# Optimization experiments

Hardware: AMD Instinct MI355X
Metric: run time of the kernel (lower is better)

The kernel has to match this reference:

```python
import jax, jax.numpy as jnp
import numpy as np


def _lstm(x, W_ih, W_hh, b_ih, b_hh):
    """PyTorch-semantics LSTM over [B, T, F] -> [B, T, H]. Gate order: i, f, g, o."""
    H = W_hh.shape[1]
    # Precompute input projection for all timesteps: [B, T, 4H]
    xg = jnp.einsum('btf,gf->btg', x, W_ih) + b_ih + b_hh
    xg = jnp.transpose(xg, (1, 0, 2))  # time-major [T, B, 4H]
    B = x.shape[0]
    h0 = jnp.zeros((B, H), dtype=x.dtype)
    c0 = jnp.zeros((B, H), dtype=x.dtype)

    def step(carry, xt):
        h, c = carry
        gates = xt + h @ W_hh.T  # [B, 4H]
        i, f, g, o = jnp.split(gates, 4, axis=-1)
        i = jax.nn.sigmoid(i)
        f = jax.nn.sigmoid(f)
        g = jnp.tanh(g)
        o = jax.nn.sigmoid(o)
        c = f * c + i * g
        h = o * jnp.tanh(c)
        return (h, c), h

    _, hs = jax.lax.scan(step, (h0, c0), xg)
    return jnp.transpose(hs, (1, 0, 2))  # [B, T, H]


def setup_inputs() -> dict:
    key = jax.random.key(0)
    ks = jax.random.split(key, 16)
    B, T, F = 4096, 256, 32
    H1, H2, D1 = 64, 32, 16
    s1 = 1.0 / np.sqrt(H1)
    s2 = 1.0 / np.sqrt(H2)
    inp = {
        'x': jax.random.normal(ks[0], (B, T, F), dtype=jnp.float32),
        'W_ih1': jax.random.uniform(ks[1], (4 * H1, F), jnp.float32, -s1, s1),
        'W_hh1': jax.random.uniform(ks[2], (4 * H1, H1), jnp.float32, -s1, s1),
        'b_ih1': jax.random.uniform(ks[3], (4 * H1,), jnp.float32, -s1, s1),
        'b_hh1': jax.random.uniform(ks[4], (4 * H1,), jnp.float32, -s1, s1),
        'W_ih2': jax.random.uniform(ks[5], (4 * H2, H1), jnp.float32, -s2, s2),
        'W_hh2': jax.random.uniform(ks[6], (4 * H2, H2), jnp.float32, -s2, s2),
        'b_ih2': jax.random.uniform(ks[7], (4 * H2,), jnp.float32, -s2, s2),
        'b_hh2': jax.random.uniform(ks[8], (4 * H2,), jnp.float32, -s2, s2),
        'W_fc1': jax.random.uniform(ks[9], (D1, H2), jnp.float32, -s2, s2),
        'b_fc1': jax.random.uniform(ks[10], (D1,), jnp.float32, -s2, s2),
        'W_fc2': jax.random.uniform(ks[11], (1, D1), jnp.float32, -0.25, 0.25),
        'b_fc2': jax.random.uniform(ks[12], (1,), jnp.float32, -0.25, 0.25),
    }
    return inp


def reference(x, W_ih1, W_hh1, b_ih1, b_hh1, W_ih2, W_hh2, b_ih2, b_hh2,
              W_fc1, b_fc1, W_fc2, b_fc2):
    # Dropout is identity in eval/inference mode.
    h = _lstm(x, W_ih1, W_hh1, b_ih1, b_hh1)        # [B, T, 64]
    h = _lstm(h, W_ih2, W_hh2, b_ih2, b_hh2)        # [B, T, 32]
    h = h[:, -1, :]                                  # [B, 32]
    h = jax.nn.relu(h @ W_fc1.T + b_fc1)             # [B, 16]
    out = h @ W_fc2.T + b_fc2                        # [B, 1]
    return out.squeeze(-1)                           # [B]
```

## Files before the change

kernel.cpp:

```cpp
#include <hip/hip_runtime.h>

#define T_   256
#define F_   32
#define NBB  16
#define TPB  768
#define IMW  136
#define XLW  40
#define PR1  260
#define PR2  132

typedef __attribute__((ext_vector_type(8))) short bf16x8;
typedef __attribute__((ext_vector_type(4))) float f32x4;
typedef __attribute__((ext_vector_type(4))) unsigned short ush4;

#define K1f  (-1.44269504f)
#define K2f  (-2.88539008f)

__device__ __forceinline__ unsigned short bf16_rne(float x){
    unsigned u = __float_as_uint(x);
    u += 0x7FFF + ((u >> 16) & 1);
    return (unsigned short)(u >> 16);
}
__device__ __forceinline__ void bf16_split(float x, unsigned short& h, unsigned short& l){
    h = bf16_rne(x);
    float xr = __uint_as_float(((unsigned)h) << 16);
    l = bf16_rne(x - xr);
}
__device__ __forceinline__ void make_frags_s(const float* __restrict__ p8, float s,
                                             bf16x8& fh, bf16x8& fl){
    #pragma unroll
    for (int e = 0; e < 8; ++e){
        unsigned short h, l; bf16_split(s * p8[e], h, l);
        fh[e] = (short)h; fl[e] = (short)l;
    }
}
__device__ __forceinline__ float sigm_pre(float p){
    return __builtin_amdgcn_rcpf(1.f + __builtin_amdgcn_exp2f(p));
}
__device__ __forceinline__ float tanh_pre(float p){
    return fmaf(2.f, __builtin_amdgcn_rcpf(1.f + __builtin_amdgcn_exp2f(p)), -1.f);
}
__device__ __forceinline__ float unit_combine(float gi, float gf, float gg, float go, float& c){
    const float i_ = sigm_pre(gi);
    const float f_ = sigm_pre(gf);
    const float g_ = tanh_pre(gg);
    const float o_ = sigm_pre(go);
    c = fmaf(f_, c, i_ * g_);
    return o_ * tanh_pre(K2f * c);
}

#define MFMA(A,B,C) __builtin_amdgcn_mfma_f32_16x16x32_bf16((A),(B),(C),0,0,0)

__device__ __forceinline__ void step_barrier(){
    asm volatile("s_waitcnt lgkmcnt(0)" ::: "memory");
    __builtin_amdgcn_s_barrier();
}

__global__ __launch_bounds__(TPB, 3) void lstm_mfma(
    const float* __restrict__ x,
    const float* __restrict__ W_ih1,
    const float* __restrict__ W_hh1,
    const float* __restrict__ b_ih1,
    const float* __restrict__ b_hh1,
    const float* __restrict__ W_ih2,
    const float* __restrict__ W_hh2,
    const float* __restrict__ b_ih2,
    const float* __restrict__ b_hh2,
    const float* __restrict__ W_fc1,
    const float* __restrict__ b_fc1,
    const float* __restrict__ W_fc2,
    const float* __restrict__ b_fc2,
    float* __restrict__ out)
{
    const int tid  = threadIdx.x;
    const int lane = tid & 63;
    const int wid  = tid >> 6;
    const int bb   = lane & 15;
    const int kg   = (lane >> 4) & 3;
    const int b0   = blockIdx.x * NBB;

    __shared__ __align__(16) unsigned short i12[2][NBB][IMW];
    __shared__ __align__(16) unsigned short x1l[2][NBB][XLW];
    __shared__ __align__(16) float pre1[NBB * PR1];
    __shared__ __align__(16) float pre2[NBB * PR2];
    __shared__ float hfin[NBB][32];
    __shared__ float hd[NBB][16];

    bf16x8 wh[2][3], wl[2][3];
    f32x4  bfr[2];
    int    offs[2];
    if (wid < 8){
        #pragma unroll
        for (int tt = 0; tt < 2; ++tt){
            const int Tt = 2*wid + tt;
            const int g = Tt >> 2, rb = Tt & 3;
            const float s = (g == 2) ? K2f : K1f;
            offs[tt] = 64*g + 16*rb;
            const int r = offs[tt] + bb;
            make_frags_s(&W_ih1[r*32 +      8*kg], s, wh[tt][0], wl[tt][0]);
            make_frags_s(&W_hh1[r*64 +      8*kg], s, wh[tt][1], wl[tt][1]);
            make_frags_s(&W_hh1[r*64 + 32 + 8*kg], s, wh[tt][2], wl[tt][2]);
            #pragma unroll
            for (int q = 0; q < 4; ++q){
                const int row = offs[tt] + 4*kg + q;
                bfr[tt][q] = s * (b_ih1[row] + b_hh1[row]);
            }
        }
    } else {
        const int j = wid - 8;
        #pragma unroll
        for (int tt = 0; tt < 2; ++tt){
            const int St = 2*j + tt;
            const int g = St >> 1, rb = St & 1;
            const float s = (g == 2) ? K2f : K1f;
            offs[tt] = 32*g + 16*rb;
            const int r = offs[tt] + bb;
            make_frags_s(&W_ih2[r*64 +      8*kg], s, wh[tt][0], wl[tt][0]);
            make_frags_s(&W_ih2[r*64 + 32 + 8*kg], s, wh[tt][1], wl[tt][1]);
            make_frags_s(&W_hh2[r*32 +      8*kg], s, wh[tt][2], wl[tt][2]);
            #pragma unroll
            for (int q = 0; q < 4; ++q){
                const int row = offs[tt] + 4*kg + q;
                bfr[tt][q] = s * (b_ih2[row] + b_hh2[row]);
            }
        }
    }

    const int cb = tid >> 4;
    const int u0 = (tid & 15) * 4;
    float c1[4] = {0.f, 0.f, 0.f, 0.f};
    const int c2t = tid & 127;
    const int cb2 = c2t >> 3;
    const int v0  = (c2t & 7) * 4;
    float c2[4] = {0.f, 0.f, 0.f, 0.f};
    const int xt  = tid & 127;
    const int xcb = xt >> 3;
    const int xf  = (xt & 7) * 4;
    const size_t xbase = (size_t)(b0 + xcb) * (T_*F_) + xf;
    float4 xc = make_float4(0.f, 0.f, 0.f, 0.f);

    for (int i = tid; i < 2*NBB*IMW; i += TPB) (&i12[0][0][0])[i] = 0;
    __syncthreads();
    if (wid >= 10){
        float4 x0 = *(const float4*)&x[xbase];
        ush4 HH, HL;
        unsigned short h, l;
        bf16_split(x0.x, h, l); HH[0]=h; HL[0]=l;
        bf16_split(x0.y, h, l); HH[1]=h; HL[1]=l;
        bf16_split(x0.z, h, l); HH[2]=h; HL[2]=l;
        bf16_split(x0.w, h, l); HH[3]=h; HL[3]=l;
        *(ush4*)&i12[0][xcb][xf] = HH;
        *(ush4*)&x1l[0][xcb][xf] = HL;
        xc = *(const float4*)&x[xbase + F_];
    }
    __syncthreads();

    for (int t = 0; t <= T_ + 1; ++t){
        const int cur = t & 1, nxt = cur ^ 1;

        if (wid < 8){
            if (t < T_){
                const unsigned short* ph = &i12[cur][0][0] + bb*IMW + 8*kg;
                bf16x8 vh[3];
                #pragma unroll
                for (int kb = 0; kb < 3; ++kb)
                    vh[kb] = *(const bf16x8*)(ph + 32*kb);
                const bf16x8 vl0 = *(const bf16x8*)&x1l[cur][bb][8*kg];
                __builtin_amdgcn_s_setprio(1);
                f32x4 a0 = bfr[0], a1 = bfr[1];
                #pragma unroll
                for (int kb = 0; kb < 3; ++kb){
                    a0 = MFMA(wh[0][kb], vh[kb], a0);
                    a1 = MFMA(wh[1][kb], vh[kb], a1);
                }
                #pragma unroll
                for (int kb = 0; kb < 3; ++kb){
                    a0 = MFMA(wl[0][kb], vh[kb], a0);
                    a1 = MFMA(wl[1][kb], vh[kb], a1);
                }
                a0 = MFMA(wh[0][0], vl0, a0);
                a1 = MFMA(wh[1][0], vl0, a1);
                __builtin_amdgcn_s_setprio(0);
                *(f32x4*)&pre1[bb*PR1 + offs[0] + 4*kg] = a0;
                *(f32x4*)&pre1[bb*PR1 + offs[1] + 4*kg] = a1;
            }
        } else if (wid < 10){
            const int m = t - 2;
            if (m >= 0 && m < T_){
                const float* p = &pre2[cb2*PR2];
                const f32x4 gi = *(const f32x4*)&p[     v0];
                const f32x4 gf = *(const f32x4*)&p[32 + v0];
                const f32x4 gg = *(const f32x4*)&p[64 + v0];
                const f32x4 go = *(const f32x4*)&p[96 + v0];
                ush4 HH;
                float hv[4];
                #pragma unroll
                for (int q = 0; q < 4; ++q){
                    hv[q] = unit_combine(gi[q], gf[q], gg[q], go[q], c2[q]);
                    HH[q] = bf16_rne(hv[q]);
                }
                *(ush4*)&i12[cur][cb2][96 + v0] = HH;
                if (m == T_ - 1){
                    hfin[cb2][v0]   = hv[0]; hfin[cb2][v0+1] = hv[1];
                    hfin[cb2][v0+2] = hv[2]; hfin[cb2][v0+3] = hv[3];
                }
            }
        } else {
            if (t + 1 < T_){
                ush4 HH, HL;
                unsigned short h, l;
                bf16_split(xc.x, h, l); HH[0]=h; HL[0]=l;
                bf16_split(xc.y, h, l); HH[1]=h; HL[1]=l;
                bf16_split(xc.z, h, l); HH[2]=h; HL[2]=l;
                bf16_split(xc.w, h, l); HH[3]=h; HL[3]=l;
                *(ush4*)&i12[nxt][xcb][xf] = HH;
                *(ush4*)&x1l[nxt][xcb][xf] = HL;
                const int tn = (t + 2 < T_) ? t + 2 : T_ - 1;
                xc = *(const float4*)&x[xbase + (size_t)tn * F_];
            }
        }
        step_barrier();

        if (wid < 4){
            if (t < T_){
                const float* p = &pre1[cb*PR1];
                const f32x4 gi = *(const f32x4*)&p[      u0];
                const f32x4 gf = *(const f32x4*)&p[ 64 + u0];
                const f32x4 gg = *(const f32x4*)&p[128 + u0];
                const f32x4 go = *(const f32x4*)&p[192 + u0];
                ush4 HH;
                #pragma unroll
                for (int q = 0; q < 4; ++q){
                    const float h = unit_combine(gi[q], gf[q], gg[q], go[q], c1[q]);
                    HH[q] = bf16_rne(h);
                }
                *(ush4*)&i12[nxt][cb][32 + u0] = HH;
            }
        } else if (wid >= 8){
            const int k = t - 1;
            if (k >= 0 && k < T_){
                const unsigned short* ph = &i12[cur][0][0] + bb*IMW + 32 + 8*kg;
                bf16x8 vh[3];
                #pragma unroll
                for (int kb = 0; kb < 3; ++kb)
                    vh[kb] = *(const bf16x8*)(ph + 32*kb);
                __builtin_amdgcn_s_setprio(1);
                f32x4 a0 = bfr[0], a1 = bfr[1];
                #pragma unroll
                for (int kb = 0; kb < 3; ++kb){
                    a0 = MFMA(wh[0][kb], vh[kb], a0);
                    a1 = MFMA(wh[1][kb], vh[kb], a1);
                }
                #pragma unroll
                for (int kb = 0; kb < 3; ++kb){
                    a0 = MFMA(wl[0][kb], vh[kb], a0);
                    a1 = MFMA(wl[1][kb], vh[kb], a1);
                }
                __builtin_amdgcn_s_setprio(0);
                *(f32x4*)&pre2[bb*PR2 + offs[0] + 4*kg] = a0;
                *(f32x4*)&pre2[bb*PR2 + offs[1] + 4*kg] = a1;
            }
        }
        step_barrier();
    }

    __syncthreads();
    if (tid < NBB * 16){
        const int b = tid >> 4, j2 = tid & 15;
        float a = b_fc1[j2];
        #pragma unroll
        for (int kk = 0; kk < 32; ++kk) a = fmaf(W_fc1[j2*32 + kk], hfin[b][kk], a);
        hd[b][j2] = fmaxf(a, 0.f);
    }
    __syncthreads();
    if (tid < NBB){
        float a = b_fc2[0];
        #pragma unroll
        for (int kk = 0; kk < 16; ++kk) a = fmaf(W_fc2[kk], hd[tid][kk], a);
        out[b0 + tid] = a;
    }
}

extern "C" void kernel_launch(void* const* d_in, const int* in_sizes, int n_in,
                              void* d_out, int out_size, void* d_ws, size_t ws_size,
                              hipStream_t stream) {
    const float* x     = (const float*)d_in[0];
    const float* W_ih1 = (const float*)d_in[1];
    const float* W_hh1 = (const float*)d_in[2];
    const float* b_ih1 = (const float*)d_in[3];
    const float* b_hh1 = (const float*)d_in[4];
    const float* W_ih2 = (const float*)d_in[5];
    const float* W_hh2 = (const float*)d_in[6];
    const float* b_ih2 = (const float*)d_in[7];
    const float* b_hh2 = (const float*)d_in[8];
    const float* W_fc1 = (const float*)d_in[9];
    const float* b_fc1 = (const float*)d_in[10];
    const float* W_fc2 = (const float*)d_in[11];
    const float* b_fc2 = (const float*)d_in[12];
    float* out = (float*)d_out;

    const int B = in_sizes[0] / (T_ * F_);
    dim3 grid(B / NBB), block(TPB);
    hipLaunchKernelGGL(lstm_mfma, grid, block, 0, stream,
                       x, W_ih1, W_hh1, b_ih1, b_hh1,
                       W_ih2, W_hh2, b_ih2, b_hh2,
                       W_fc1, b_fc1, W_fc2, b_fc2, out);
}
```

Measured before the change: 248.0 us.

## Fuse gate combine into MFMA waves, one barrier per step

Each MFMA wave now computes all four gates (i,f,g,o) for its 16 hidden units and applies the cell update directly from accumulator registers. This removes the pre1/pre2 shared-memory staging, the separate combine waves, and the second barrier of each timestep. The block shrinks from 12 to 8 waves and the pipeline drops one stage. In exchange, each wave holds twice as many weight fragments in registers, occupancy is lowered to 2 blocks, and the gate math now sits serially after the MFMAs on the critical path.

```diff
diff --git a/kernel.cpp b/kernel.cpp
--- a/kernel.cpp
+++ b/kernel.cpp
@@ -3,11 +3,9 @@
 #define T_   256
 #define F_   32
 #define NBB  16
-#define TPB  768
+#define TPB  512
 #define IMW  136
 #define XLW  40
-#define PR1  260
-#define PR2  132
 
 typedef __attribute__((ext_vector_type(8))) short bf16x8;
 typedef __attribute__((ext_vector_type(4))) float f32x4;
@@ -56,7 +54,7 @@
     __builtin_amdgcn_s_barrier();
 }
 
-__global__ __launch_bounds__(TPB, 3) void lstm_mfma(
+__global__ __launch_bounds__(TPB, 2) void lstm_mfma(
     const float* __restrict__ x,
     const float* __restrict__ W_ih1,
     const float* __restrict__ W_hh1,
@@ -81,58 +79,44 @@
 
     __shared__ __align__(16) unsigned short i12[2][NBB][IMW];
     __shared__ __align__(16) unsigned short x1l[2][NBB][XLW];
-    __shared__ __align__(16) float pre1[NBB * PR1];
-    __shared__ __align__(16) float pre2[NBB * PR2];
     __shared__ float hfin[NBB][32];
     __shared__ float hd[NBB][16];
 
-    bf16x8 wh[2][3], wl[2][3];
-    f32x4  bfr[2];
-    int    offs[2];
-    if (wid < 8){
-        #pragma unroll
-        for (int tt = 0; tt < 2; ++tt){
-            const int Tt = 2*wid + tt;
-            const int g = Tt >> 2, rb = Tt & 3;
+    bf16x8 wh[4][3], wl[4][3];
+    f32x4  bfr[4];
+    if (wid < 4){
+        #pragma unroll
+        for (int g = 0; g < 4; ++g){
             const float s = (g == 2) ? K2f : K1f;
-            offs[tt] = 64*g + 16*rb;
-            const int r = offs[tt] + bb;
-            make_frags_s(&W_ih1[r*32 +      8*kg], s, wh[tt][0], wl[tt][0]);
-            make_frags_s(&W_hh1[r*64 +      8*kg], s, wh[tt][1], wl[tt][1]);
-            make_frags_s(&W_hh1[r*64 + 32 + 8*kg], s, wh[tt][2], wl[tt][2]);
+            const int r = 64*g + 16*wid + bb;
+            make_frags_s(&W_ih1[r*32 +      8*kg], s, wh[g][0], wl[g][0]);
+            make_frags_s(&W_hh1[r*64 +      8*kg], s, wh[g][1], wl[g][1]);
+            make_frags_s(&W_hh1[r*64 + 32 + 8*kg], s, wh[g][2], wl[g][2]);
             #pragma unroll
             for (int q = 0; q < 4; ++q){
-                const int row = offs[tt] + 4*kg + q;
-                bfr[tt][q] = s * (b_ih1[row] + b_hh1[row]);
+                const int row = 64*g + 16*wid + 4*kg + q;
+                bfr[g][q] = s * (b_ih1[row] + b_hh1[row]);
             }
         }
-    } else {
-        const int j = wid - 8;
-        #pragma unroll
-        for (int tt = 0; tt < 2; ++tt){
-            const int St = 2*j + tt;
-            const int g = St >> 1, rb = St & 1;
+    } else if (wid < 6){
+        const int j = wid - 4;
+        #pragma unroll
+        for (int g = 0; g < 4; ++g){
             const float s = (g == 2) ? K2f : K1f;
-            offs[tt] = 32*g + 16*rb;
-            const int r = offs[tt] + bb;
-            make_frags_s(&W_ih2[r*64 +      8*kg], s, wh[tt][0], wl[tt][0]);
-            make_frags_s(&W_ih2[r*64 + 32 + 8*kg], s, wh[tt][1], wl[tt][1]);
-            make_frags_s(&W_hh2[r*32 +      8*kg], s, wh[tt][2], wl[tt][2]);
+            const int r = 32*g + 16*j + bb;
+            make_frags_s(&W_ih2[r*64 +      8*kg], s, wh[g][0], wl[g][0]);
+            make_frags_s(&W_ih2[r*64 + 32 + 8*kg], s, wh[g][1], wl[g][1]);
+            make_frags_s(&W_hh2[r*32 +      8*kg], s, wh[g][2], wl[g][2]);
             #pragma unroll
             for (int q = 0; q < 4; ++q){
-                const int row = offs[tt] + 4*kg + q;
-                bfr[tt][q] = s * (b_ih2[row] + b_hh2[row]);
+                const int row = 32*g + 16*j + 4*kg + q;
+                bfr[g][q] = s * (b_ih2[row] + b_hh2[row]);
             }
         }
     }
 
-    const int cb = tid >> 4;
-    const int u0 = (tid & 15) * 4;
-    float c1[4] = {0.f, 0.f, 0.f, 0.f};
-    const int c2t = tid & 127;
-    const int cb2 = c2t >> 3;
-    const int v0  = (c2t & 7) * 4;
-    float c2[4] = {0.f, 0.f, 0.f, 0.f};
+    float cc[4] = {0.f, 0.f, 0.f, 0.f};
+
     const int xt  = tid & 127;
     const int xcb = xt >> 3;
     const int xf  = (xt & 7) * 4;
@@ -141,7 +125,7 @@
 
     for (int i = tid; i < 2*NBB*IMW; i += TPB) (&i12[0][0][0])[i] = 0;
     __syncthreads();
-    if (wid >= 10){
+    if (wid >= 6){
         float4 x0 = *(const float4*)&x[xbase];
         ush4 HH, HL;
         unsigned short h, l;
@@ -155,10 +139,10 @@
     }
     __syncthreads();
 
-    for (int t = 0; t <= T_ + 1; ++t){
+    for (int t = 0; t <= T_; ++t){
         const int cur = t & 1, nxt = cur ^ 1;
 
-        if (wid < 8){
+        if (wid < 4){
             if (t < T_){
                 const unsigned short* ph = &i12[cur][0][0] + bb*IMW + 8*kg;
                 bf16x8 vh[3];
@@ -167,42 +151,71 @@
                     vh[kb] = *(const bf16x8*)(ph + 32*kb);
                 const bf16x8 vl0 = *(const bf16x8*)&x1l[cur][bb][8*kg];
                 __builtin_amdgcn_s_setprio(1);
-                f32x4 a0 = bfr[0], a1 = bfr[1];
+                f32x4 a0 = bfr[0], a1 = bfr[1], a2 = bfr[2], a3 = bfr[3];
                 #pragma unroll
                 for (int kb = 0; kb < 3; ++kb){
                     a0 = MFMA(wh[0][kb], vh[kb], a0);
                     a1 = MFMA(wh[1][kb], vh[kb], a1);
+                    a2 = MFMA(wh[2][kb], vh[kb], a2);
+                    a3 = MFMA(wh[3][kb], vh[kb], a3);
                 }
                 #pragma unroll
                 for (int kb = 0; kb < 3; ++kb){
                     a0 = MFMA(wl[0][kb], vh[kb], a0);
                     a1 = MFMA(wl[1][kb], vh[kb], a1);
+                    a2 = MFMA(wl[2][kb], vh[kb], a2);
+                    a3 = MFMA(wl[3][kb], vh[kb], a3);
                 }
                 a0 = MFMA(wh[0][0], vl0, a0);
                 a1 = MFMA(wh[1][0], vl0, a1);
+                a2 = MFMA(wh[2][0], vl0, a2);
+                a3 = MFMA(wh[3][0], vl0, a3);
                 __builtin_amdgcn_s_setprio(0);
-                *(f32x4*)&pre1[bb*PR1 + offs[0] + 4*kg] = a0;
-                *(f32x4*)&pre1[bb*PR1 + offs[1] + 4*kg] = a1;
-            }
-        } else if (wid < 10){
-            const int m = t - 2;
-            if (m >= 0 && m < T_){
-                const float* p = &pre2[cb2*PR2];
-                const f32x4 gi = *(const f32x4*)&p[     v0];
-                const f32x4 gf = *(const f32x4*)&p[32 + v0];
-                const f32x4 gg = *(const f32x4*)&p[64 + v0];
-                const f32x4 go = *(const f32x4*)&p[96 + v0];
+                ush4 HH;
+                #pragma unroll
+                for (int q = 0; q < 4; ++q){
+                    const float h = unit_combine(a0[q], a1[q], a2[q], a3[q], cc[q]);
+                    HH[q] = bf16_rne(h);
+                }
+                *(ush4*)&i12[nxt][bb][32 + 16*wid + 4*kg] = HH;
+            }
+        } else if (wid < 6){
+            if (t >= 1){
+                const unsigned short* ph = &i12[cur][0][0] + bb*IMW + 32 + 8*kg;
+                bf16x8 vh[3];
+                #pragma unroll
+                for (int kb = 0; kb < 3; ++kb)
+                    vh[kb] = *(const bf16x8*)(ph + 32*kb);
+                __builtin_amdgcn_s_setprio(1);
+                f32x4 a0 = bfr[0], a1 = bfr[1], a2 = bfr[2], a3 = bfr[3];
+                #pragma unroll
+                for (int kb = 0; kb < 3; ++kb){
+                    a0 = MFMA(wh[0][kb], vh[kb], a0);
+                    a1 = MFMA(wh[1][kb], vh[kb], a1);
+                    a2 = MFMA(wh[2][kb], vh[kb], a2);
+                    a3 = MFMA(wh[3][kb], vh[kb], a3);
+                }
+                #pragma unroll
+                for (int kb = 0; kb < 3; ++kb){
+                    a0 = MFMA(wl[0][kb], vh[kb], a0);
+                    a1 = MFMA(wl[1][kb], vh[kb], a1);
+                    a2 = MFMA(wl[2][kb], vh[kb], a2);
+                    a3 = MFMA(wl[3][kb], vh[kb], a3);
+                }
+                __builtin_amdgcn_s_setprio(0);
+                const int j = wid - 4;
                 ush4 HH;
                 float hv[4];
                 #pragma unroll
                 for (int q = 0; q < 4; ++q){
-                    hv[q] = unit_combine(gi[q], gf[q], gg[q], go[q], c2[q]);
+                    hv[q] = unit_combine(a0[q], a1[q], a2[q], a3[q], cc[q]);
                     HH[q] = bf16_rne(hv[q]);
                 }
-                *(ush4*)&i12[cur][cb2][96 + v0] = HH;
-                if (m == T_ - 1){
-                    hfin[cb2][v0]   = hv[0]; hfin[cb2][v0+1] = hv[1];
-                    hfin[cb2][v0+2] = hv[2]; hfin[cb2][v0+3] = hv[3];
+                *(ush4*)&i12[nxt][bb][96 + 16*j + 4*kg] = HH;
+                if (t - 1 == T_ - 1){
+                    const int u = 16*j + 4*kg;
+                    hfin[bb][u]   = hv[0]; hfin[bb][u+1] = hv[1];
+                    hfin[bb][u+2] = hv[2]; hfin[bb][u+3] = hv[3];
                 }
             }
         } else {
@@ -217,48 +230,6 @@
                 *(ush4*)&x1l[nxt][xcb][xf] = HL;
                 const int tn = (t + 2 < T_) ? t + 2 : T_ - 1;
                 xc = *(const float4*)&x[xbase + (size_t)tn * F_];
-            }
-        }
-        step_barrier();
-
-        if (wid < 4){
-            if (t < T_){
-                const float* p = &pre1[cb*PR1];
-                const f32x4 gi = *(const f32x4*)&p[      u0];
-                const f32x4 gf = *(const f32x4*)&p[ 64 + u0];
-                const f32x4 gg = *(const f32x4*)&p[128 + u0];
-                const f32x4 go = *(const f32x4*)&p[192 + u0];
-                ush4 HH;
-                #pragma unroll
-                for (int q = 0; q < 4; ++q){
-                    const float h = unit_combine(gi[q], gf[q], gg[q], go[q], c1[q]);
-                    HH[q] = bf16_rne(h);
-                }
-                *(ush4*)&i12[nxt][cb][32 + u0] = HH;
-            }
-        } else if (wid >= 8){
-            const int k = t - 1;
-            if (k >= 0 && k < T_){
-                const unsigned short* ph = &i12[cur][0][0] + bb*IMW + 32 + 8*kg;
-                bf16x8 vh[3];
-                #pragma unroll
-                for (int kb = 0; kb < 3; ++kb)
-                    vh[kb] = *(const bf16x8*)(ph + 32*kb);
-                __builtin_amdgcn_s_setprio(1);
-                f32x4 a0 = bfr[0], a1 = bfr[1];
-                #pragma unroll
-                for (int kb = 0; kb < 3; ++kb){
-                    a0 = MFMA(wh[0][kb], vh[kb], a0);
-                    a1 = MFMA(wh[1][kb], vh[kb], a1);
-                }
-                #pragma unroll
-                for (int kb = 0; kb < 3; ++kb){
-                    a0 = MFMA(wl[0][kb], vh[kb], a0);
-                    a1 = MFMA(wl[1][kb], vh[kb], a1);
-                }
-                __builtin_amdgcn_s_setprio(0);
-                *(f32x4*)&pre2[bb*PR2 + offs[0] + 4*kg] = a0;
-                *(f32x4*)&pre2[bb*PR2 + offs[1] + 4*kg] = a1;
             }
         }
         step_barrier();
```

Result: faster. 236.9 us (-4.5%).
